# Kernel optimization log

Measured on AMD Instinct MI355X. Metric: run time of the kernel, lower is better.

Reference implementation:

```python
import jax, jax.numpy as jnp
import numpy as np

NUM_GRAPHS = 64


def setup_inputs() -> dict:
    key = jax.random.key(0)
    ks = jax.random.split(key, 8)
    N, E, H, D_IN, NEXP = 100000, 1600000, 128, 4, 8
    atomic_numbers = jax.random.uniform(ks[0], (N,), dtype=jnp.float32) * 80.0
    pos = jax.random.normal(ks[1], (N, 3), dtype=jnp.float32)
    W0 = jax.random.normal(ks[2], (D_IN, H), dtype=jnp.float32) / np.sqrt(D_IN)
    b0 = jnp.zeros((H,), dtype=jnp.float32)
    W1 = jax.random.normal(ks[3], (H, H), dtype=jnp.float32) / np.sqrt(H)
    b1 = jnp.zeros((H,), dtype=jnp.float32)
    W2 = jax.random.normal(ks[4], (H, H), dtype=jnp.float32) / np.sqrt(H)
    b2 = jnp.zeros((H,), dtype=jnp.float32)
    lin_W = jax.random.normal(ks[5], (H, NEXP), dtype=jnp.float32) / np.sqrt(H)
    lin_b = jnp.zeros((NEXP,), dtype=jnp.float32)
    edge_index = jax.random.randint(ks[6], (2, E), 0, N, dtype=jnp.int64)
    batch = jnp.sort(jax.random.randint(ks[7], (N,), 0, NUM_GRAPHS, dtype=jnp.int64))
    return {
        "atomic_numbers": atomic_numbers, "pos": pos,
        "W0": W0, "b0": b0, "W1": W1, "b1": b1, "W2": W2, "b2": b2,
        "lin_W": lin_W, "lin_b": lin_b,
        "edge_index": edge_index, "batch": batch,
    }


def _gcn_layer(x, W, b, src, dst, norm, num_nodes):
    # GCNConv: transform, then symmetric-normalized scatter-aggregate (self-loops included in src/dst)
    h = x @ W                                   # [N, H]
    msg = h[src] * norm[:, None]                # [E+N, H] edge-gather
    out = jax.ops.segment_sum(msg, dst, num_segments=num_nodes)  # scatter-add at targets
    return out + b


def reference(atomic_numbers, pos, W0, b0, W1, b1, W2, b2, lin_W, lin_b, edge_index, batch):
    N = atomic_numbers.shape[0]
    x = jnp.concatenate([atomic_numbers[:, None], pos], axis=-1)  # [N, 4]

    # add self-loops (PyG GCNConv default)
    loop = jnp.arange(N, dtype=edge_index.dtype)
    src = jnp.concatenate([edge_index[0], loop])
    dst = jnp.concatenate([edge_index[1], loop])
    deg = jax.ops.segment_sum(jnp.ones_like(dst, dtype=jnp.float32), dst, num_segments=N)
    deg_inv_sqrt = jnp.where(deg > 0, deg ** -0.5, 0.0)
    norm = deg_inv_sqrt[src] * deg_inv_sqrt[dst]  # [E+N]

    for (W, b) in ((W0, b0), (W1, b1), (W2, b2)):
        x = _gcn_layer(x, W, b, src, dst, norm, N)
        x = jax.nn.relu(x)
        # dropout is identity at inference

    # global mean pool over graphs
    sums = jax.ops.segment_sum(x, batch, num_segments=NUM_GRAPHS)        # [G, H]
    counts = jax.ops.segment_sum(jnp.ones((N,), jnp.float32), batch, num_segments=NUM_GRAPHS)
    pooled = sums / jnp.maximum(counts, 1.0)[:, None]

    logits = pooled @ lin_W + lin_b             # [G, num_experts]
    return jax.nn.softmax(logits, axis=1)[:, :, None]  # [G, num_experts, 1]
```

## Files before the change

kernel.cpp:

```cpp
#include <hip/hip_runtime.h>
#include <math.h>

#define WG 256
#define NB 256
#define BSHIFT 9
#define NBLK 256

typedef float vf2 __attribute__((ext_vector_type(2)));
typedef short bf16x8 __attribute__((ext_vector_type(8)));
typedef float f32x4 __attribute__((ext_vector_type(4)));

#define XS_STRIDE 136
#define WT_STRIDE 136
#define C_STRIDE 132

__device__ __forceinline__ int lower_bound_i(const int* __restrict__ a, int n, int key) {
    int lo = 0, hi = n;
    while (lo < hi) { int mid = (lo + hi) >> 1; if (a[mid] < key) lo = mid + 1; else hi = mid; }
    return lo;
}

__device__ __forceinline__ void fp8x8_to_f8(uint2 raw, float* f) {
    vf2 a = __builtin_amdgcn_cvt_pk_f32_fp8((int)raw.x, false);
    vf2 b = __builtin_amdgcn_cvt_pk_f32_fp8((int)raw.x, true);
    vf2 c = __builtin_amdgcn_cvt_pk_f32_fp8((int)raw.y, false);
    vf2 d = __builtin_amdgcn_cvt_pk_f32_fp8((int)raw.y, true);
    f[0]=a.x; f[1]=a.y; f[2]=b.x; f[3]=b.y; f[4]=c.x; f[5]=c.y; f[6]=d.x; f[7]=d.y;
}
__device__ __forceinline__ void fp8x16_to_f(uint4 raw, float* f) {
    uint2 lo, hi;
    lo.x = raw.x; lo.y = raw.y; hi.x = raw.z; hi.y = raw.w;
    fp8x8_to_f8(lo, f);
    fp8x8_to_f8(hi, f + 8);
}
__device__ __forceinline__ unsigned int f4_to_fp8x4(float x, float y, float z, float w) {
    int v = __builtin_amdgcn_cvt_pk_fp8_f32(x, y, 0, false);
    v = __builtin_amdgcn_cvt_pk_fp8_f32(z, w, v, true);
    return (unsigned int)v;
}
__device__ __forceinline__ unsigned short f_to_bf_trunc(float f) {
    return (unsigned short)(__float_as_uint(f) >> 16);
}
__device__ __forceinline__ unsigned short f_to_bf_rne(float f) {
    unsigned int u = __float_as_uint(f);
    u += 0x7FFFu + ((u >> 16) & 1u);
    return (unsigned short)(u >> 16);
}


__global__ __launch_bounds__(256) void k_cnt(const int* __restrict__ edst, int E,
                                             int* __restrict__ gcounts) {
    __shared__ int hist[NB];
    int t = threadIdx.x, blk = blockIdx.x;
    if (t < NB) hist[t] = 0;
    __syncthreads();
    int chunk = (E + NBLK - 1) / NBLK;
    int e0 = blk * chunk, e1 = min(E, e0 + chunk);
    for (int e = e0 + t; e < e1; e += 256) atomicAdd(&hist[edst[e] >> BSHIFT], 1);
    __syncthreads();
    if (t < NB) gcounts[t * NBLK + blk] = hist[t];
}

__global__ __launch_bounds__(256) void k_scanA(int* __restrict__ gcounts,
                                               int* __restrict__ bsum) {
    __shared__ int wtot[4];
    int t = threadIdx.x;
    int base = blockIdx.x * 1024 + t * 4;
    int4 v = *(const int4*)&gcounts[base];
    int s = v.x + v.y + v.z + v.w;
    int lane = t & 63, wid = t >> 6;
    int x = s;
#pragma unroll
    for (int d = 1; d < 64; d <<= 1) { int y = __shfl_up(x, d); if (lane >= d) x += y; }
    if (lane == 63) wtot[wid] = x;
    __syncthreads();
    int woff = 0;
    for (int w = 0; w < wid; w++) woff += wtot[w];
    int excl = woff + x - s;
    int4 o;
    o.x = excl; o.y = excl + v.x; o.z = o.y + v.y; o.w = o.z + v.z;
    *(int4*)&gcounts[base] = o;
    if (t == 255) bsum[blockIdx.x] = woff + x;
}

__global__ void k_scanB(int* __restrict__ bsum) {
    int t = threadIdx.x;
    int v = bsum[t];
    int x = v;
#pragma unroll
    for (int d = 1; d < 64; d <<= 1) { int y = __shfl_up(x, d); if (t >= d) x += y; }
    bsum[t] = x - v;
}

__global__ __launch_bounds__(256) void k_scat(const int* __restrict__ esrc,
        const int* __restrict__ edst, int E,
        const int* __restrict__ gcounts, const int* __restrict__ bsum,
        int* __restrict__ pairs) {
    __shared__ int cur[NB];
    int t = threadIdx.x, blk = blockIdx.x;
    if (t < NB) {
        int idx = t * NBLK + blk;
        cur[t] = gcounts[idx] + bsum[idx >> 10];
    }
    __syncthreads();
    int chunk = (E + NBLK - 1) / NBLK;
    int e0 = blk * chunk, e1 = min(E, e0 + chunk);
    for (int e = e0 + t; e < e1; e += 256) {
        int d = edst[e], s = esrc[e];
        int pos = atomicAdd(&cur[d >> BSHIFT], 1);
        pairs[pos] = (s << BSHIFT) | (d & ((1 << BSHIFT) - 1));
    }
}

__global__ __launch_bounds__(256) void k_build(const int* __restrict__ pairs,
        const int* __restrict__ gcounts, const int* __restrict__ bsum, int N, int E,
        int* __restrict__ offs, int* __restrict__ srcs, float* __restrict__ dis) {
    __shared__ int cnt[512];
    __shared__ int wtot[4];
    int b = blockIdx.x, t = threadIdx.x;
    int n0 = b << BSHIFT;
    cnt[2 * t] = 0; cnt[2 * t + 1] = 0;
    __syncthreads();
    int i0 = b * NBLK, i1 = (b + 1) * NBLK;
    int bs = gcounts[i0] + bsum[i0 >> 10];
    int be = gcounts[i1] + bsum[i1 >> 10];
    int m = be - bs;
    const int* pb = &pairs[bs];
    for (int i = t; i < m; i += 256) {
        int p = pb[i];
        atomicAdd(&cnt[p & 511], 1);
    }
    __syncthreads();
    int v0 = cnt[2 * t], v1 = cnt[2 * t + 1];
    int ts = v0 + v1;
    int lane = t & 63, wid = t >> 6;
    int x = ts;
    #pragma unroll
    for (int d = 1; d < 64; d <<= 1) { int y = __shfl_up(x, d); if (lane >= d) x += y; }
    if (lane == 63) wtot[wid] = x;
    __syncthreads();
    int woff = 0;
    for (int w = 0; w < wid; w++) woff += wtot[w];
    int excl = woff + x - ts;
    int o0 = excl, o1 = excl + v0;
    cnt[2 * t] = o0; cnt[2 * t + 1] = o1;
    int n = n0 + 2 * t;
    if (n + 0 < N) { offs[n + 0] = bs + o0; dis[n + 0] = rsqrtf((float)(v0 + 1)); }
    if (n + 1 < N) { offs[n + 1] = bs + o1; dis[n + 1] = rsqrtf((float)(v1 + 1)); }
    if (b == gridDim.x - 1 && t == 255) offs[N] = E;
    __syncthreads();
    for (int i = t; i < m; i += 256) {
        int p = pb[i];
        int pos = atomicAdd(&cnt[p & 511], 1);
        srcs[bs + pos] = p >> BSHIFT;
    }
}

__global__ __launch_bounds__(256) void k_wt(const float* __restrict__ W,
                                            unsigned short* __restrict__ wt) {
    int idx = blockIdx.x * 256 + threadIdx.x;
    int k = idx >> 7, j = idx & 127;
    float v = W[k * 128 + j];
    wt[j * 128 + k] = f_to_bf_rne(v);
}


__global__ void k_y(const float* __restrict__ an, const float* __restrict__ pos,
                    const float* __restrict__ dis, float4* __restrict__ y, int N) {
    int n = blockIdx.x * blockDim.x + threadIdx.x;
    if (n >= N) return;
    float dn = dis[n];
    float4 v;
    v.x = dn * an[n];
    v.y = dn * pos[n * 3 + 0];
    v.z = dn * pos[n * 3 + 1];
    v.w = dn * pos[n * 3 + 2];
    y[n] = v;
}

__global__ __launch_bounds__(256) void k_agg0t(const float4* __restrict__ y,
        const float* __restrict__ W0, const float* __restrict__ b0,
        const float* __restrict__ dis, const int* __restrict__ offs,
        const int* __restrict__ srcs, unsigned int* __restrict__ h, int N) {
    int n = blockIdx.x * blockDim.x + threadIdx.x;
    if (n >= N) return;
    float4 acc = y[n];
    int e0 = offs[n], e1 = offs[n + 1];
    int e = e0;
    for (; e + 4 <= e1; e += 4) {
        float4 r0 = y[srcs[e + 0]];
        float4 r1 = y[srcs[e + 1]];
        float4 r2 = y[srcs[e + 2]];
        float4 r3 = y[srcs[e + 3]];
        acc.x += (r0.x + r1.x) + (r2.x + r3.x);
        acc.y += (r0.y + r1.y) + (r2.y + r3.y);
        acc.z += (r0.z + r1.z) + (r2.z + r3.z);
        acc.w += (r0.w + r1.w) + (r2.w + r3.w);
    }
    for (; e < e1; ++e) {
        float4 r = y[srcs[e]];
        acc.x += r.x; acc.y += r.y; acc.z += r.z; acc.w += r.w;
    }
    float dn = dis[n];
    acc.x *= dn; acc.y *= dn; acc.z *= dn; acc.w *= dn;
#pragma unroll
    for (int c = 0; c < 8; c++) {
        float o[16];
#pragma unroll
        for (int q = 0; q < 4; q++) {
            const float4 bq = *(const float4*)&b0[c * 16 + q * 4];
            const float4 w0q = *(const float4*)&W0[0 * 128 + c * 16 + q * 4];
            const float4 w1q = *(const float4*)&W0[1 * 128 + c * 16 + q * 4];
            const float4 w2q = *(const float4*)&W0[2 * 128 + c * 16 + q * 4];
            const float4 w3q = *(const float4*)&W0[3 * 128 + c * 16 + q * 4];
            o[q*4+0] = fmaxf(bq.x + acc.x*w0q.x + acc.y*w1q.x + acc.z*w2q.x + acc.w*w3q.x, 0.f);
            o[q*4+1] = fmaxf(bq.y + acc.x*w0q.y + acc.y*w1q.y + acc.z*w2q.y + acc.w*w3q.y, 0.f);
            o[q*4+2] = fmaxf(bq.z + acc.x*w0q.z + acc.y*w1q.z + acc.z*w2q.z + acc.w*w3q.z, 0.f);
            o[q*4+3] = fmaxf(bq.w + acc.x*w0q.w + acc.y*w1q.w + acc.z*w2q.w + acc.w*w3q.w, 0.f);
        }
        uint4 outv;
        outv.x = f4_to_fp8x4(o[0], o[1], o[2], o[3]);
        outv.y = f4_to_fp8x4(o[4], o[5], o[6], o[7]);
        outv.z = f4_to_fp8x4(o[8], o[9], o[10], o[11]);
        outv.w = f4_to_fp8x4(o[12], o[13], o[14], o[15]);
        *(uint4*)&h[(size_t)n * 32 + c * 4] = outv;
    }
}

__global__ __launch_bounds__(256) void k_gemm(const unsigned int* __restrict__ x,
                                              const unsigned short* __restrict__ wt,
                                              const float* __restrict__ dis,
                                              unsigned int* __restrict__ h, int N) {
    __shared__ __align__(16) char ldsb[(64 * XS_STRIDE + 128 * WT_STRIDE) * 2];
    unsigned short* xs  = (unsigned short*)ldsb;
    unsigned short* wtl = xs + 64 * XS_STRIDE;
    float* Cs = (float*)ldsb;

    int t = threadIdx.x;
    int n0 = blockIdx.x * 64;

    {
        const uint2* xg = (const uint2*)(x + (size_t)n0 * 32);
        int validq = min(64, N - n0) * 16;
#pragma unroll
        for (int i = 0; i < 4; i++) {
            int idx = t + i * 256;
            int row = idx >> 4, part = idx & 15;
            float f[8];
            if (idx < validq) {
                fp8x8_to_f8(xg[idx], f);
#pragma unroll
                for (int k = 0; k < 8; k++) f[k] = fmaxf(f[k], 0.f);
            } else {
#pragma unroll
                for (int k = 0; k < 8; k++) f[k] = 0.f;
            }
            bf16x8 v;
#pragma unroll
            for (int k = 0; k < 8; k++) v[k] = (short)f_to_bf_trunc(f[k]);
            *(bf16x8*)&xs[row * XS_STRIDE + part * 8] = v;
        }
    }
    {
        const uint4* wg = (const uint4*)wt;
#pragma unroll
        for (int i = 0; i < 8; i++) {
            int idx = t + i * 256;
            int j = idx >> 4, part = idx & 15;
            uint4 v = wg[idx];
            *(uint4*)&wtl[j * WT_STRIDE + part * 8] = v;
        }
    }
    __syncthreads();

    int lane = t & 63, wv = t >> 6;
    int m = lane & 15, quad = lane >> 4;
    int rowbase = wv * 16;

    f32x4 acc[8];
#pragma unroll
    for (int c = 0; c < 8; c++) acc[c] = (f32x4){0.f, 0.f, 0.f, 0.f};

#pragma unroll
    for (int kt = 0; kt < 4; kt++) {
        bf16x8 a = *(bf16x8*)&xs[(rowbase + m) * XS_STRIDE + kt * 32 + quad * 8];
#pragma unroll
        for (int c = 0; c < 8; c++) {
            bf16x8 b = *(bf16x8*)&wtl[(c * 16 + m) * WT_STRIDE + kt * 32 + quad * 8];
            acc[c] = __builtin_amdgcn_mfma_f32_16x16x32_bf16(a, b, acc[c], 0, 0, 0);
        }
    }
    __syncthreads();

#pragma unroll
    for (int c = 0; c < 8; c++) {
#pragma unroll
        for (int r = 0; r < 4; r++) {
            Cs[(rowbase + quad * 4 + r) * C_STRIDE + c * 16 + m] = acc[c][r];
        }
    }
    __syncthreads();

    int fq = t & 31, ng = t >> 5;
#pragma unroll
    for (int i = 0; i < 8; i++) {
        int lrow = ng * 8 + i;
        int n = n0 + lrow;
        if (n < N) {
            float4 v = *(const float4*)&Cs[lrow * C_STRIDE + 4 * fq];
            float dn = dis[n];
            h[(size_t)n * 32 + fq] = f4_to_fp8x4(v.x * dn, v.y * dn, v.z * dn, v.w * dn);
        }
    }
}

__global__ __launch_bounds__(256) void k_agg(const unsigned int* __restrict__ h,
                      const float* __restrict__ bias,
                      const float* __restrict__ dis, const int* __restrict__ offs,
                      const int* __restrict__ srcs, unsigned int* __restrict__ agg, int N) {
    int fq = threadIdx.x & 7, ng = threadIdx.x >> 3;
    int n = blockIdx.x * 32 + ng;
    if (n >= N) return;
    const uint4* hp4 = (const uint4*)h;
    float acc[16], tmp[16];
    fp8x16_to_f(hp4[(size_t)n * 8 + fq], acc);
    int e0 = offs[n], e1 = offs[n + 1];
    int e = e0;
    for (; e + 8 <= e1; e += 8) {
        uint4 r0 = hp4[(size_t)srcs[e + 0] * 8 + fq];
        uint4 r1 = hp4[(size_t)srcs[e + 1] * 8 + fq];
        uint4 r2 = hp4[(size_t)srcs[e + 2] * 8 + fq];
        uint4 r3 = hp4[(size_t)srcs[e + 3] * 8 + fq];
        uint4 r4 = hp4[(size_t)srcs[e + 4] * 8 + fq];
        uint4 r5 = hp4[(size_t)srcs[e + 5] * 8 + fq];
        uint4 r6 = hp4[(size_t)srcs[e + 6] * 8 + fq];
        uint4 r7 = hp4[(size_t)srcs[e + 7] * 8 + fq];
        fp8x16_to_f(r0, tmp);
#pragma unroll
        for (int k = 0; k < 16; k++) acc[k] += tmp[k];
        fp8x16_to_f(r1, tmp);
#pragma unroll
        for (int k = 0; k < 16; k++) acc[k] += tmp[k];
        fp8x16_to_f(r2, tmp);
#pragma unroll
        for (int k = 0; k < 16; k++) acc[k] += tmp[k];
        fp8x16_to_f(r3, tmp);
#pragma unroll
        for (int k = 0; k < 16; k++) acc[k] += tmp[k];
        fp8x16_to_f(r4, tmp);
#pragma unroll
        for (int k = 0; k < 16; k++) acc[k] += tmp[k];
        fp8x16_to_f(r5, tmp);
#pragma unroll
        for (int k = 0; k < 16; k++) acc[k] += tmp[k];
        fp8x16_to_f(r6, tmp);
#pragma unroll
        for (int k = 0; k < 16; k++) acc[k] += tmp[k];
        fp8x16_to_f(r7, tmp);
#pragma unroll
        for (int k = 0; k < 16; k++) acc[k] += tmp[k];
    }
    for (; e + 4 <= e1; e += 4) {
        uint4 r0 = hp4[(size_t)srcs[e + 0] * 8 + fq];
        uint4 r1 = hp4[(size_t)srcs[e + 1] * 8 + fq];
        uint4 r2 = hp4[(size_t)srcs[e + 2] * 8 + fq];
        uint4 r3 = hp4[(size_t)srcs[e + 3] * 8 + fq];
        fp8x16_to_f(r0, tmp);
#pragma unroll
        for (int k = 0; k < 16; k++) acc[k] += tmp[k];
        fp8x16_to_f(r1, tmp);
#pragma unroll
        for (int k = 0; k < 16; k++) acc[k] += tmp[k];
        fp8x16_to_f(r2, tmp);
#pragma unroll
        for (int k = 0; k < 16; k++) acc[k] += tmp[k];
        fp8x16_to_f(r3, tmp);
#pragma unroll
        for (int k = 0; k < 16; k++) acc[k] += tmp[k];
    }
    for (; e < e1; ++e) {
        fp8x16_to_f(hp4[(size_t)srcs[e] * 8 + fq], tmp);
#pragma unroll
        for (int k = 0; k < 16; k++) acc[k] += tmp[k];
    }
    float dn = dis[n];
    float bv[16];
    *(float4*)&bv[0]  = *(const float4*)&bias[fq * 16 + 0];
    *(float4*)&bv[4]  = *(const float4*)&bias[fq * 16 + 4];
    *(float4*)&bv[8]  = *(const float4*)&bias[fq * 16 + 8];
    *(float4*)&bv[12] = *(const float4*)&bias[fq * 16 + 12];
    float o[16];
#pragma unroll
    for (int k = 0; k < 16; k++) o[k] = bv[k] + dn * acc[k];
    uint4 outv;
    outv.x = f4_to_fp8x4(o[0], o[1], o[2], o[3]);
    outv.y = f4_to_fp8x4(o[4], o[5], o[6], o[7]);
    outv.z = f4_to_fp8x4(o[8], o[9], o[10], o[11]);
    outv.w = f4_to_fp8x4(o[12], o[13], o[14], o[15]);
    *(uint4*)&agg[(size_t)n * 32 + fq * 4] = outv;
}


__global__ void k_pool(const unsigned int* __restrict__ x, const int* __restrict__ batch,
                       float* __restrict__ pooled, int N) {
    int g = blockIdx.x >> 3, c = blockIdx.x & 7;
    int start = lower_bound_i(batch, N, g);
    int end   = lower_bound_i(batch, N, g + 1);
    int len = end - start;
    int cb = start + (int)((long)len * c / 8);
    int ce = start + (int)((long)len * (c + 1) / 8);
    int fq = threadIdx.x & 31, rg = threadIdx.x >> 5;
    float acc[4] = {0.f, 0.f, 0.f, 0.f};
    for (int n = cb + rg; n < ce; n += 8) {
        unsigned int u = x[(size_t)n * 32 + fq];
        vf2 lo = __builtin_amdgcn_cvt_pk_f32_fp8((int)u, false);
        vf2 hi = __builtin_amdgcn_cvt_pk_f32_fp8((int)u, true);
        acc[0] += fmaxf(lo.x, 0.f); acc[1] += fmaxf(lo.y, 0.f);
        acc[2] += fmaxf(hi.x, 0.f); acc[3] += fmaxf(hi.y, 0.f);
    }
    __shared__ float sh[8 * 128];
#pragma unroll
    for (int k = 0; k < 4; k++) sh[rg * 128 + fq * 4 + k] = acc[k];
    __syncthreads();
    int t = threadIdx.x;
    if (t < 128) {
        float s = 0.f;
#pragma unroll
        for (int r = 0; r < 8; r++) s += sh[r * 128 + t];
        atomicAdd(&pooled[g * 128 + t], s);
    }
}

__global__ void k_head(const float* __restrict__ pooled, const int* __restrict__ batch,
                       const float* __restrict__ linW, const float* __restrict__ linb,
                       float* __restrict__ out, int N) {
    int g = threadIdx.x;
    if (g >= 64) return;
    int start = lower_bound_i(batch, N, g);
    int end   = lower_bound_i(batch, N, g + 1);
    float cnt = fmaxf((float)(end - start), 1.0f);
    float logits[8];
#pragma unroll
    for (int j = 0; j < 8; j++) logits[j] = linb[j];
    for (int f = 0; f < 128; f++) {
        float p = pooled[g * 128 + f] / cnt;
#pragma unroll
        for (int j = 0; j < 8; j++) logits[j] += p * linW[f * 8 + j];
    }
    float m = logits[0];
#pragma unroll
    for (int j = 1; j < 8; j++) m = fmaxf(m, logits[j]);
    float s = 0.f;
    float e[8];
#pragma unroll
    for (int j = 0; j < 8; j++) { e[j] = expf(logits[j] - m); s += e[j]; }
#pragma unroll
    for (int j = 0; j < 8; j++) out[g * 8 + j] = e[j] / s;
}


extern "C" void kernel_launch(void* const* d_in, const int* in_sizes, int n_in,
                              void* d_out, int out_size, void* d_ws, size_t ws_size,
                              hipStream_t stream) {
    const float* an   = (const float*)d_in[0];
    const float* pos  = (const float*)d_in[1];
    const float* W0   = (const float*)d_in[2];
    const float* b0   = (const float*)d_in[3];
    const float* W1   = (const float*)d_in[4];
    const float* b1   = (const float*)d_in[5];
    const float* W2   = (const float*)d_in[6];
    const float* b2   = (const float*)d_in[7];
    const float* linW = (const float*)d_in[8];
    const float* linb = (const float*)d_in[9];
    const int*   ei   = (const int*)d_in[10];
    const int*   batch= (const int*)d_in[11];

    int N = in_sizes[0];
    int E = in_sizes[10] / 2;
    const int* esrc = ei;
    const int* edst = ei + E;
    int nb = (N + (1 << BSHIFT) - 1) >> BSHIFT;

    char* p = (char*)d_ws;
    auto carve = [&](size_t bytes) -> void* {
        void* r = (void*)p;
        p += (bytes + 255) & ~(size_t)255;
        return r;
    };
    unsigned int* bufA = (unsigned int*)carve((size_t)N * 128);
    unsigned int* bufB = (unsigned int*)carve((size_t)N * 128);
    float* dis    = (float*)carve((size_t)N * 4);
    float4* ybuf  = (float4*)carve((size_t)N * 16);
    int*   offs   = (int*)  carve((size_t)(N + 1) * 4);
    int*   srcs   = (int*)  carve((size_t)E * 4);
    int*   pairs  = (int*)  carve((size_t)E * 4);
    int*   gcounts= (int*)  carve((size_t)NB * NBLK * 4);
    int*   bsum   = (int*)  carve(64 * 4);
    unsigned short* wt1 = (unsigned short*)carve(128 * 128 * 2);
    unsigned short* wt2 = (unsigned short*)carve(128 * 128 * 2);
    float* pooled = (float*)carve(64 * 128 * 4);

    hipMemsetAsync(pooled, 0, 64 * 128 * 4, stream);

    k_cnt  <<<NBLK, WG, 0, stream>>>(edst, E, gcounts);
    k_scanA<<<(NB * NBLK) / 1024, WG, 0, stream>>>(gcounts, bsum);
    k_scanB<<<1, 64, 0, stream>>>(bsum);
    k_scat <<<NBLK, WG, 0, stream>>>(esrc, edst, E, gcounts, bsum, pairs);
    k_build<<<nb, WG, 0, stream>>>(pairs, gcounts, bsum, N, E, offs, srcs, dis);

    k_wt<<<64, WG, 0, stream>>>(W1, wt1);
    k_wt<<<64, WG, 0, stream>>>(W2, wt2);

    k_y    <<<(N + WG - 1) / WG, WG, 0, stream>>>(an, pos, dis, ybuf, N);
    k_agg0t<<<(N + WG - 1) / WG, WG, 0, stream>>>(ybuf, W0, b0, dis, offs, srcs, bufA, N);
    k_gemm<<<(N + 63) / 64, WG, 0, stream>>>(bufA, wt1, dis, bufB, N);
    k_agg <<<(N + 31) / 32, WG, 0, stream>>>(bufB, b1, dis, offs, srcs, bufA, N);
    k_gemm<<<(N + 63) / 64, WG, 0, stream>>>(bufA, wt2, dis, bufB, N);
    k_agg <<<(N + 31) / 32, WG, 0, stream>>>(bufB, b2, dis, offs, srcs, bufA, N);

    k_pool<<<64 * 8, WG, 0, stream>>>(bufA, batch, pooled, N);
    k_head<<<1, 64, 0, stream>>>(pooled, batch, linW, linb, (float*)d_out, N);
}
```

Baseline: 295.4 us.

## Process nodes in degree-sorted order in aggregation kernels and fuse k_y into k_build

Adds a counting sort of nodes by in-degree (histogram, scan, scatter kernels) that produces a permutation, and the aggregation kernels now take their node from that permutation. Threads in a wavefront then have similar edge counts, which is meant to cut divergence and load imbalance. The separate k_y kernel is folded into k_build to save a launch and a pass over memory. The cost is three extra small kernels, an extra indirection, and output writes that are no longer contiguous across neighbouring threads.

```diff
diff --git a/kernel.cpp b/kernel.cpp
--- a/kernel.cpp
+++ b/kernel.cpp
@@ -5,6 +5,7 @@
 #define NB 256
 #define BSHIFT 9
 #define NBLK 256
+#define DB 64
 
 typedef float vf2 __attribute__((ext_vector_type(2)));
 typedef short bf16x8 __attribute__((ext_vector_type(8)));
@@ -114,7 +115,9 @@
 
 __global__ __launch_bounds__(256) void k_build(const int* __restrict__ pairs,
         const int* __restrict__ gcounts, const int* __restrict__ bsum, int N, int E,
-        int* __restrict__ offs, int* __restrict__ srcs, float* __restrict__ dis) {
+        const float* __restrict__ an, const float* __restrict__ pos,
+        int* __restrict__ offs, int* __restrict__ srcs, float* __restrict__ dis,
+        int* __restrict__ deg, float4* __restrict__ y) {
     __shared__ int cnt[512];
     __shared__ int wtot[4];
     int b = blockIdx.x, t = threadIdx.x;
@@ -136,7 +139,7 @@
     int lane = t & 63, wid = t >> 6;
     int x = ts;
     #pragma unroll
-    for (int d = 1; d < 64; d <<= 1) { int y = __shfl_up(x, d); if (lane >= d) x += y; }
+    for (int d = 1; d < 64; d <<= 1) { int y2 = __shfl_up(x, d); if (lane >= d) x += y2; }
     if (lane == 63) wtot[wid] = x;
     __syncthreads();
     int woff = 0;
@@ -145,14 +148,78 @@
     int o0 = excl, o1 = excl + v0;
     cnt[2 * t] = o0; cnt[2 * t + 1] = o1;
     int n = n0 + 2 * t;
-    if (n + 0 < N) { offs[n + 0] = bs + o0; dis[n + 0] = rsqrtf((float)(v0 + 1)); }
-    if (n + 1 < N) { offs[n + 1] = bs + o1; dis[n + 1] = rsqrtf((float)(v1 + 1)); }
+    if (n + 0 < N) {
+        float dn = rsqrtf((float)(v0 + 1));
+        offs[n + 0] = bs + o0; dis[n + 0] = dn; deg[n + 0] = v0;
+        float4 v;
+        v.x = dn * an[n]; v.y = dn * pos[n * 3 + 0];
+        v.z = dn * pos[n * 3 + 1]; v.w = dn * pos[n * 3 + 2];
+        y[n + 0] = v;
+    }
+    if (n + 1 < N) {
+        float dn = rsqrtf((float)(v1 + 1));
+        offs[n + 1] = bs + o1; dis[n + 1] = dn; deg[n + 1] = v1;
+        float4 v;
+        v.x = dn * an[n + 1]; v.y = dn * pos[(n + 1) * 3 + 0];
+        v.z = dn * pos[(n + 1) * 3 + 1]; v.w = dn * pos[(n + 1) * 3 + 2];
+        y[n + 1] = v;
+    }
     if (b == gridDim.x - 1 && t == 255) offs[N] = E;
     __syncthreads();
     for (int i = t; i < m; i += 256) {
         int p = pb[i];
-        int pos = atomicAdd(&cnt[p & 511], 1);
-        srcs[bs + pos] = p >> BSHIFT;
+        int pos2 = atomicAdd(&cnt[p & 511], 1);
+        srcs[bs + pos2] = p >> BSHIFT;
+    }
+}
+
+
+__global__ __launch_bounds__(256) void k_dhist(const int* __restrict__ deg, int N,
+                                               int* __restrict__ dh) {
+    __shared__ int hist[DB];
+    int t = threadIdx.x, blk = blockIdx.x;
+    if (t < DB) hist[t] = 0;
+    __syncthreads();
+    int chunk = (N + 255) / 256;
+    int n0 = blk * chunk, n1 = min(N, n0 + chunk);
+    for (int n = n0 + t; n < n1; n += 256) atomicAdd(&hist[min(deg[n], DB - 1)], 1);
+    __syncthreads();
+    if (t < DB) dh[t * 256 + blk] = hist[t];
+}
+
+__global__ __launch_bounds__(256) void k_dscan(int* __restrict__ dh) {
+    __shared__ int wtot[4];
+    int t = threadIdx.x;
+    int base = t * 64;
+    int s = 0;
+    for (int i = 0; i < 64; i++) s += dh[base + i];
+    int lane = t & 63, wid = t >> 6;
+    int x = s;
+#pragma unroll
+    for (int d = 1; d < 64; d <<= 1) { int y = __shfl_up(x, d); if (lane >= d) x += y; }
+    if (lane == 63) wtot[wid] = x;
+    __syncthreads();
+    int woff = 0;
+    for (int w = 0; w < wid; w++) woff += wtot[w];
+    int run = woff + x - s;
+    for (int i = 0; i < 64; i++) {
+        int v = dh[base + i];
+        dh[base + i] = run;
+        run += v;
+    }
+}
+
+__global__ __launch_bounds__(256) void k_dscat(const int* __restrict__ deg, int N,
+        const int* __restrict__ dh, int* __restrict__ perm) {
+    __shared__ int cur[DB];
+    int t = threadIdx.x, blk = blockIdx.x;
+    if (t < DB) cur[t] = dh[t * 256 + blk];
+    __syncthreads();
+    int chunk = (N + 255) / 256;
+    int n0 = blk * chunk, n1 = min(N, n0 + chunk);
+    for (int n = n0 + t; n < n1; n += 256) {
+        int pos = atomicAdd(&cur[min(deg[n], DB - 1)], 1);
+        perm[pos] = n;
     }
 }
 
@@ -165,25 +232,14 @@
 }
 
 
-__global__ void k_y(const float* __restrict__ an, const float* __restrict__ pos,
-                    const float* __restrict__ dis, float4* __restrict__ y, int N) {
-    int n = blockIdx.x * blockDim.x + threadIdx.x;
-    if (n >= N) return;
-    float dn = dis[n];
-    float4 v;
-    v.x = dn * an[n];
-    v.y = dn * pos[n * 3 + 0];
-    v.z = dn * pos[n * 3 + 1];
-    v.w = dn * pos[n * 3 + 2];
-    y[n] = v;
-}
-
 __global__ __launch_bounds__(256) void k_agg0t(const float4* __restrict__ y,
         const float* __restrict__ W0, const float* __restrict__ b0,
         const float* __restrict__ dis, const int* __restrict__ offs,
-        const int* __restrict__ srcs, unsigned int* __restrict__ h, int N) {
-    int n = blockIdx.x * blockDim.x + threadIdx.x;
-    if (n >= N) return;
+        const int* __restrict__ srcs, const int* __restrict__ perm,
+        unsigned int* __restrict__ h, int N) {
+    int idx = blockIdx.x * blockDim.x + threadIdx.x;
+    if (idx >= N) return;
+    int n = perm[idx];
     float4 acc = y[n];
     int e0 = offs[n], e1 = offs[n + 1];
     int e = e0;
@@ -317,10 +373,12 @@
 __global__ __launch_bounds__(256) void k_agg(const unsigned int* __restrict__ h,
                       const float* __restrict__ bias,
                       const float* __restrict__ dis, const int* __restrict__ offs,
-                      const int* __restrict__ srcs, unsigned int* __restrict__ agg, int N) {
+                      const int* __restrict__ srcs, const int* __restrict__ perm,
+                      unsigned int* __restrict__ agg, int N) {
     int fq = threadIdx.x & 7, ng = threadIdx.x >> 3;
-    int n = blockIdx.x * 32 + ng;
-    if (n >= N) return;
+    int idx = blockIdx.x * 32 + ng;
+    if (idx >= N) return;
+    int n = perm[idx];
     const uint4* hp4 = (const uint4*)h;
     float acc[16], tmp[16];
     fp8x16_to_f(hp4[(size_t)n * 8 + fq], acc);
@@ -491,11 +549,14 @@
     unsigned int* bufB = (unsigned int*)carve((size_t)N * 128);
     float* dis    = (float*)carve((size_t)N * 4);
     float4* ybuf  = (float4*)carve((size_t)N * 16);
+    int*   deg    = (int*)  carve((size_t)N * 4);
+    int*   perm   = (int*)  carve((size_t)N * 4);
     int*   offs   = (int*)  carve((size_t)(N + 1) * 4);
     int*   srcs   = (int*)  carve((size_t)E * 4);
     int*   pairs  = (int*)  carve((size_t)E * 4);
     int*   gcounts= (int*)  carve((size_t)NB * NBLK * 4);
     int*   bsum   = (int*)  carve(64 * 4);
+    int*   dh     = (int*)  carve((size_t)DB * 256 * 4);
     unsigned short* wt1 = (unsigned short*)carve(128 * 128 * 2);
     unsigned short* wt2 = (unsigned short*)carve(128 * 128 * 2);
     float* pooled = (float*)carve(64 * 128 * 4);
@@ -506,17 +567,21 @@
     k_scanA<<<(NB * NBLK) / 1024, WG, 0, stream>>>(gcounts, bsum);
     k_scanB<<<1, 64, 0, stream>>>(bsum);
     k_scat <<<NBLK, WG, 0, stream>>>(esrc, edst, E, gcounts, bsum, pairs);
-    k_build<<<nb, WG, 0, stream>>>(pairs, gcounts, bsum, N, E, offs, srcs, dis);
+    k_build<<<nb, WG, 0, stream>>>(pairs, gcounts, bsum, N, E, an, pos,
+                                   offs, srcs, dis, deg, ybuf);
+
+    k_dhist<<<256, WG, 0, stream>>>(deg, N, dh);
+    k_dscan<<<1, WG, 0, stream>>>(dh);
+    k_dscat<<<256, WG, 0, stream>>>(deg, N, dh, perm);
 
     k_wt<<<64, WG, 0, stream>>>(W1, wt1);
     k_wt<<<64, WG, 0, stream>>>(W2, wt2);
 
-    k_y    <<<(N + WG - 1) / WG, WG, 0, stream>>>(an, pos, dis, ybuf, N);
-    k_agg0t<<<(N + WG - 1) / WG, WG, 0, stream>>>(ybuf, W0, b0, dis, offs, srcs, bufA, N);
+    k_agg0t<<<(N + WG - 1) / WG, WG, 0, stream>>>(ybuf, W0, b0, dis, offs, srcs, perm, bufA, N);
     k_gemm<<<(N + 63) / 64, WG, 0, stream>>>(bufA, wt1, dis, bufB, N);
-    k_agg <<<(N + 31) / 32, WG, 0, stream>>>(bufB, b1, dis, offs, srcs, bufA, N);
+    k_agg <<<(N + 31) / 32, WG, 0, stream>>>(bufB, b1, dis, offs, srcs, perm, bufA, N);
     k_gemm<<<(N + 63) / 64, WG, 0, stream>>>(bufA, wt2, dis, bufB, N);
-    k_agg <<<(N + 31) / 32, WG, 0, stream>>>(bufB, b2, dis, offs, srcs, bufA, N);
+    k_agg <<<(N + 31) / 32, WG, 0, stream>>>(bufB, b2, dis, offs, srcs, perm, bufA, N);
 
     k_pool<<<64 * 8, WG, 0, stream>>>(bufA, batch, pooled, N);
     k_head<<<1, 64, 0, stream>>>(pooled, batch, linW, linb, (float*)d_out, N);
```

New measurement: 306.6 us. 3.8% more time.
